# Kernel tuning notes

Hardware: AMD Instinct MI355X
Metric: run time of the kernel (lower is better)

The kernel has to match this reference:

```python
import jax, jax.numpy as jnp
import numpy as np

TOP_K = 2
EPS = 1e-10


def setup_inputs() -> dict:
    key = jax.random.key(0)
    k1, k2 = jax.random.split(key)
    B, S, D, E = 4, 4096, 4096, 64
    hidden_states = jax.random.normal(k1, (B, S, D), dtype=jnp.float32)
    # router weight, scaled like a standard linear init
    w_router = jax.random.normal(k2, (D, E), dtype=jnp.float32) / np.sqrt(D)
    return {"hidden_states": hidden_states, "w_router": w_router}


def reference(hidden_states, w_router):
    # router: [B,S,D] x [D,E] -> [B,S,E]
    router_logits = jnp.einsum("bsd,de->bse", hidden_states, w_router)
    # balanced_assignment: softmax, global load, penalty, adjusted top-k
    routing_probs = jax.nn.softmax(router_logits, axis=-1)
    current_load = routing_probs.sum(axis=(0, 1))            # [E]
    load_penalty = current_load / (current_load.mean() + EPS)  # [E]
    adjusted_logits = router_logits - jnp.log(load_penalty + EPS)
    _, expert_indices = jax.lax.top_k(adjusted_logits, TOP_K)  # [B,S,top_k]
    return adjusted_logits, expert_indices
```

## Files before the change

kernel.cpp:

```cpp
#include <hip/hip_runtime.h>
#include <math.h>

#define ROWS 16384
#define DD   4096
#define EE   64
#define EPSF 1e-10f

#define BM     128
#define KT     32
#define KSPLIT 4
#define KRANGE (DD / KSPLIT)
#define NKT    (KRANGE / KT)
#define WTILE  12288

typedef __attribute__((ext_vector_type(8))) short short8;
typedef __attribute__((ext_vector_type(4))) float f32x4;
typedef __attribute__((ext_vector_type(4))) unsigned u32x4;

__device__ __forceinline__ void split3x8(const float f[8], u32x4& w0,
                                         u32x4& w1, u32x4& w2) {
#pragma unroll
  for (int i = 0; i < 4; ++i) {
    float fa = f[2 * i], fb = f[2 * i + 1];
    unsigned ua = __float_as_uint(fa), ub = __float_as_uint(fb);
    unsigned ra = ua + 0x7fffu + ((ua >> 16) & 1u);
    unsigned rb = ub + 0x7fffu + ((ub >> 16) & 1u);
    w0[i] = (rb & 0xffff0000u) | (ra >> 16);
    fa -= __uint_as_float(ra & 0xffff0000u);
    fb -= __uint_as_float(rb & 0xffff0000u);
    ua = __float_as_uint(fa); ub = __float_as_uint(fb);
    ra = ua + 0x7fffu + ((ua >> 16) & 1u);
    rb = ub + 0x7fffu + ((ub >> 16) & 1u);
    w1[i] = (rb & 0xffff0000u) | (ra >> 16);
    fa -= __uint_as_float(ra & 0xffff0000u);
    fb -= __uint_as_float(rb & 0xffff0000u);
    ua = __float_as_uint(fa); ub = __float_as_uint(fb);
    ra = ua + 0x7fffu + ((ua >> 16) & 1u);
    rb = ub + 0x7fffu + ((ub >> 16) & 1u);
    w2[i] = (rb & 0xffff0000u) | (ra >> 16);
  }
}

__device__ __forceinline__ void dma16(const void* g, void* l) {
  __builtin_amdgcn_global_load_lds(
      (const __attribute__((address_space(1))) unsigned int*)g,
      (__attribute__((address_space(3))) unsigned int*)l, 16, 0, 0);
}

__global__ __launch_bounds__(256) void k_wsplit(const float* __restrict__ wr,
                                                unsigned char* __restrict__ out) {
  const int kt = blockIdx.x;
  const int t = threadIdx.x;
  const int lane = t & 63, wv = t >> 6;
  float f[8];
  const float* wp = wr + (size_t)(kt * 32 + wv * 8) * EE + lane;
#pragma unroll
  for (int j = 0; j < 8; ++j) f[j] = wp[(size_t)j * EE];
  u32x4 w0, w1, w2;
  split3x8(f, w0, w1, w2);
  const int et = lane >> 4;
  const int lp = wv * 16 + (lane & 15);
  unsigned char* base = out + (size_t)kt * WTILE + et * 1024 + lp * 16;
  *(u32x4*)(base + 0 * 4096) = w0;
  *(u32x4*)(base + 1 * 4096) = w1;
  *(u32x4*)(base + 2 * 4096) = w2;
}

__global__ __launch_bounds__(256) void k_gemm(
    const float* __restrict__ h, const unsigned char* __restrict__ wsp,
    float* __restrict__ logits) {
  __shared__ alignas(16) unsigned char wsf[2][WTILE];

  const int t = threadIdx.x;
  const int lane = t & 63;
  const int wv = t >> 6;
  const int row0 = (blockIdx.x >> 2) * BM;
  const int kb0 = (blockIdx.x & 3) * KRANGE;

  f32x4 acc[2][4] = {};

  const int rl0 = row0 + wv * 32 + (lane & 15);
  const int kcol = kb0 + (lane >> 4) * 8;
  const float* ap0 = h + (size_t)rl0 * DD + kcol;
  const float* ap1 = ap0 + (size_t)16 * DD;

  const unsigned char* wsrc = wsp + (size_t)(kb0 / KT) * WTILE;
  const int chunkoff = wv * 1024 + lane * 16;

  float4 cur[4], nxt[4];
  cur[0] = *(const float4*)(ap0);
  cur[1] = *(const float4*)(ap0 + 4);
  cur[2] = *(const float4*)(ap1);
  cur[3] = *(const float4*)(ap1 + 4);
#pragma unroll
  for (int c = 0; c < 3; ++c)
    dma16(wsrc + c * 4096 + chunkoff, &wsf[0][c * 4096 + chunkoff]);

  for (int kt = 0; kt < NKT; ++kt) {
    const int buf = kt & 1;
    asm volatile("s_waitcnt vmcnt(0)" ::: "memory");
    __syncthreads();

    if (kt + 1 < NKT) {
      const float* p0 = ap0 + (size_t)(kt + 1) * KT;
      const float* p1 = ap1 + (size_t)(kt + 1) * KT;
      nxt[0] = *(const float4*)(p0);
      nxt[1] = *(const float4*)(p0 + 4);
      nxt[2] = *(const float4*)(p1);
      nxt[3] = *(const float4*)(p1 + 4);
      const unsigned char* ws = wsrc + (size_t)(kt + 1) * WTILE;
#pragma unroll
      for (int c = 0; c < 3; ++c)
        dma16(ws + c * 4096 + chunkoff, &wsf[buf ^ 1][c * 4096 + chunkoff]);
    }

    short8 bf[3][4];
#pragma unroll
    for (int p = 0; p < 3; ++p)
#pragma unroll
      for (int et = 0; et < 4; ++et)
        bf[p][et] =
            *(const short8*)&wsf[buf][p * 4096 + et * 1024 + lane * 16];

#pragma unroll
    for (int mt = 0; mt < 2; ++mt) {
      const float4 a0 = cur[mt * 2], a1 = cur[mt * 2 + 1];
      const float af[8] = {a0.x, a0.y, a0.z, a0.w, a1.x, a1.y, a1.z, a1.w};
      u32x4 q0, q1, q2;
      split3x8(af, q0, q1, q2);
      const short8 ah0 = __builtin_bit_cast(short8, q0);
      const short8 ah1 = __builtin_bit_cast(short8, q1);
      const short8 ah2 = __builtin_bit_cast(short8, q2);
#pragma unroll
      for (int et = 0; et < 4; ++et) {
        f32x4 c = acc[mt][et];
        c = __builtin_amdgcn_mfma_f32_16x16x32_bf16(ah0, bf[0][et], c, 0, 0, 0);
        c = __builtin_amdgcn_mfma_f32_16x16x32_bf16(ah0, bf[1][et], c, 0, 0, 0);
        c = __builtin_amdgcn_mfma_f32_16x16x32_bf16(ah1, bf[0][et], c, 0, 0, 0);
        c = __builtin_amdgcn_mfma_f32_16x16x32_bf16(ah0, bf[2][et], c, 0, 0, 0);
        c = __builtin_amdgcn_mfma_f32_16x16x32_bf16(ah1, bf[1][et], c, 0, 0, 0);
        c = __builtin_amdgcn_mfma_f32_16x16x32_bf16(ah2, bf[0][et], c, 0, 0, 0);
        acc[mt][et] = c;
      }
    }

    if (kt + 1 < NKT) {
#pragma unroll
      for (int i = 0; i < 4; ++i) cur[i] = nxt[i];
    }
  }

#pragma unroll
  for (int mt = 0; mt < 2; ++mt) {
    const int rbase = row0 + wv * 32 + mt * 16 + (lane >> 4) * 4;
    const int col = lane & 15;
#pragma unroll
    for (int et = 0; et < 4; ++et) {
#pragma unroll
      for (int r = 0; r < 4; ++r)
        atomicAdd(&logits[(size_t)(rbase + r) * EE + et * 16 + col],
                  acc[mt][et][r]);
    }
  }
}

__global__ __launch_bounds__(256) void k_softload(
    const float* __restrict__ logits, float* __restrict__ g_load) {
  __shared__ float red[4][64];
  const int lane = threadIdx.x & 63;
  const int wv = threadIdx.x >> 6;
  float accp = 0.f;
#pragma unroll 4
  for (int i = 0; i < 16; ++i) {
    int row = blockIdx.x * 64 + wv * 16 + i;
    float x = logits[(size_t)row * EE + lane];
    float m = x;
#pragma unroll
    for (int off = 32; off > 0; off >>= 1) m = fmaxf(m, __shfl_xor(m, off, 64));
    float p = __expf(x - m);
    float s = p;
#pragma unroll
    for (int off = 32; off > 0; off >>= 1) s += __shfl_xor(s, off, 64);
    accp += p / s;
  }
  red[wv][lane] = accp;
  __syncthreads();
  if (wv == 0) {
    float s = red[0][lane] + red[1][lane] + red[2][lane] + red[3][lane];
    atomicAdd(&g_load[lane], s);
  }
}

__global__ __launch_bounds__(256) void k_top2(float* __restrict__ logits,
                                              const float* __restrict__ g_load,
                                              float* __restrict__ idx_out) {
  int t = threadIdx.x;
  int lane = t & 63;
  int wv = t >> 6;
  int row = blockIdx.x * 4 + wv;

  float v0 = g_load[lane];
  float s0 = v0;
#pragma unroll
  for (int off = 32; off > 0; off >>= 1) s0 += __shfl_xor(s0, off, 64);
  float lp = logf(v0 / (s0 * (1.f / 64.f) + EPSF) + EPSF);

  size_t base = (size_t)row * EE;
  float a = logits[base + lane] - lp;
  logits[base + lane] = a;

  float v = a;
  int idx = lane;
#pragma unroll
  for (int off = 32; off > 0; off >>= 1) {
    float ov = __shfl_xor(v, off, 64);
    int oi = __shfl_xor(idx, off, 64);
    if (ov > v || (ov == v && oi < idx)) { v = ov; idx = oi; }
  }
  int i1 = idx;

  float a2 = (lane == i1) ? -INFINITY : a;
  v = a2;
  idx = lane;
#pragma unroll
  for (int off = 32; off > 0; off >>= 1) {
    float ov = __shfl_xor(v, off, 64);
    int oi = __shfl_xor(idx, off, 64);
    if (ov > v || (ov == v && oi < idx)) { v = ov; idx = oi; }
  }
  int i2 = idx;

  if (lane == 0) {
    idx_out[(size_t)row * 2 + 0] = (float)i1;
    idx_out[(size_t)row * 2 + 1] = (float)i2;
  }
}

extern "C" void kernel_launch(void* const* d_in, const int* in_sizes, int n_in,
                              void* d_out, int out_size, void* d_ws,
                              size_t ws_size, hipStream_t stream) {
  const float* h = (const float*)d_in[0];
  const float* wr = (const float*)d_in[1];
  float* out = (float*)d_out;
  float* logits = out;
  float* idx_out = out + (size_t)ROWS * EE;
  float* g_load = (float*)d_ws;
  unsigned char* wsp = (unsigned char*)d_ws + 512;

  hipMemsetAsync(d_out, 0, (size_t)ROWS * EE * sizeof(float), stream);
  hipMemsetAsync(d_ws, 0, 512, stream);
  k_wsplit<<<DD / KT, 256, 0, stream>>>(wr, wsp);
  k_gemm<<<(ROWS / BM) * KSPLIT, 256, 0, stream>>>(h, wsp, logits);
  k_softload<<<ROWS / 64, 256, 0, stream>>>(logits, g_load);
  k_top2<<<ROWS / 4, 256, 0, stream>>>(logits, g_load, idx_out);
}
```

Before: 420.1 us.

## Drop split-K, fuse softmax load reduction into GEMM epilogue, remove memsets

```diff
diff --git a/kernel.cpp b/kernel.cpp
--- a/kernel.cpp
+++ b/kernel.cpp
@@ -6,12 +6,10 @@
 #define EE   64
 #define EPSF 1e-10f
 
-#define BM     128
-#define KT     32
-#define KSPLIT 4
-#define KRANGE (DD / KSPLIT)
-#define NKT    (KRANGE / KT)
-#define WTILE  12288
+#define BM    64
+#define KT    32
+#define NKT   (DD / KT)
+#define WTILE 12288
 
 typedef __attribute__((ext_vector_type(8))) short short8;
 typedef __attribute__((ext_vector_type(4))) float f32x4;
@@ -48,10 +46,12 @@
 }
 
 __global__ __launch_bounds__(256) void k_wsplit(const float* __restrict__ wr,
-                                                unsigned char* __restrict__ out) {
+                                                unsigned char* __restrict__ out,
+                                                float* __restrict__ g_load) {
   const int kt = blockIdx.x;
   const int t = threadIdx.x;
   const int lane = t & 63, wv = t >> 6;
+  if (blockIdx.x == 0 && t < 64) g_load[t] = 0.f;
   float f[8];
   const float* wp = wr + (size_t)(kt * 32 + wv * 8) * EE + lane;
 #pragma unroll
@@ -66,127 +66,112 @@
   *(u32x4*)(base + 2 * 4096) = w2;
 }
 
-__global__ __launch_bounds__(256) void k_gemm(
+__global__ __launch_bounds__(512) void k_gemm(
     const float* __restrict__ h, const unsigned char* __restrict__ wsp,
-    float* __restrict__ logits) {
-  __shared__ alignas(16) unsigned char wsf[2][WTILE];
+    float* __restrict__ logits, float* __restrict__ g_load) {
+  __shared__ alignas(16) unsigned char smem[2 * WTILE];
 
   const int t = threadIdx.x;
   const int lane = t & 63;
   const int wv = t >> 6;
-  const int row0 = (blockIdx.x >> 2) * BM;
-  const int kb0 = (blockIdx.x & 3) * KRANGE;
-
-  f32x4 acc[2][4] = {};
-
-  const int rl0 = row0 + wv * 32 + (lane & 15);
-  const int kcol = kb0 + (lane >> 4) * 8;
-  const float* ap0 = h + (size_t)rl0 * DD + kcol;
-  const float* ap1 = ap0 + (size_t)16 * DD;
-
-  const unsigned char* wsrc = wsp + (size_t)(kb0 / KT) * WTILE;
-  const int chunkoff = wv * 1024 + lane * 16;
-
-  float4 cur[4], nxt[4];
-  cur[0] = *(const float4*)(ap0);
-  cur[1] = *(const float4*)(ap0 + 4);
-  cur[2] = *(const float4*)(ap1);
-  cur[3] = *(const float4*)(ap1 + 4);
-#pragma unroll
-  for (int c = 0; c < 3; ++c)
-    dma16(wsrc + c * 4096 + chunkoff, &wsf[0][c * 4096 + chunkoff]);
+  const int mt = wv >> 1;
+  const int eh = wv & 1;
+  const int row0 = blockIdx.x * BM;
+
+  f32x4 acc[2] = {};
+
+  const float* ap =
+      h + (size_t)(row0 + mt * 16 + (lane & 15)) * DD + (lane >> 4) * 8;
+
+  const int slot0 = wv * 1024 + lane * 16;
+
+  float4 cur0, cur1, nxt0, nxt1;
+  cur0 = *(const float4*)(ap);
+  cur1 = *(const float4*)(ap + 4);
+  dma16(wsp + slot0, smem + slot0);
+  if (wv < 4) dma16(wsp + 8192 + slot0, smem + 8192 + slot0);
 
   for (int kt = 0; kt < NKT; ++kt) {
     const int buf = kt & 1;
+    const unsigned char* lb = smem + buf * WTILE;
     asm volatile("s_waitcnt vmcnt(0)" ::: "memory");
     __syncthreads();
 
     if (kt + 1 < NKT) {
-      const float* p0 = ap0 + (size_t)(kt + 1) * KT;
-      const float* p1 = ap1 + (size_t)(kt + 1) * KT;
-      nxt[0] = *(const float4*)(p0);
-      nxt[1] = *(const float4*)(p0 + 4);
-      nxt[2] = *(const float4*)(p1);
-      nxt[3] = *(const float4*)(p1 + 4);
-      const unsigned char* ws = wsrc + (size_t)(kt + 1) * WTILE;
-#pragma unroll
-      for (int c = 0; c < 3; ++c)
-        dma16(ws + c * 4096 + chunkoff, &wsf[buf ^ 1][c * 4096 + chunkoff]);
+      const float* p = ap + (size_t)(kt + 1) * KT;
+      nxt0 = *(const float4*)(p);
+      nxt1 = *(const float4*)(p + 4);
+      const unsigned char* ws = wsp + (size_t)(kt + 1) * WTILE;
+      unsigned char* nb = smem + (buf ^ 1) * WTILE;
+      dma16(ws + slot0, nb + slot0);
+      if (wv < 4) dma16(ws + 8192 + slot0, nb + 8192 + slot0);
     }
 
-    short8 bf[3][4];
+    short8 bf[3][2];
 #pragma unroll
     for (int p = 0; p < 3; ++p)
 #pragma unroll
-      for (int et = 0; et < 4; ++et)
-        bf[p][et] =
-            *(const short8*)&wsf[buf][p * 4096 + et * 1024 + lane * 16];
-
-#pragma unroll
-    for (int mt = 0; mt < 2; ++mt) {
-      const float4 a0 = cur[mt * 2], a1 = cur[mt * 2 + 1];
-      const float af[8] = {a0.x, a0.y, a0.z, a0.w, a1.x, a1.y, a1.z, a1.w};
-      u32x4 q0, q1, q2;
-      split3x8(af, q0, q1, q2);
-      const short8 ah0 = __builtin_bit_cast(short8, q0);
-      const short8 ah1 = __builtin_bit_cast(short8, q1);
-      const short8 ah2 = __builtin_bit_cast(short8, q2);
-#pragma unroll
-      for (int et = 0; et < 4; ++et) {
-        f32x4 c = acc[mt][et];
-        c = __builtin_amdgcn_mfma_f32_16x16x32_bf16(ah0, bf[0][et], c, 0, 0, 0);
-        c = __builtin_amdgcn_mfma_f32_16x16x32_bf16(ah0, bf[1][et], c, 0, 0, 0);
-        c = __builtin_amdgcn_mfma_f32_16x16x32_bf16(ah1, bf[0][et], c, 0, 0, 0);
-        c = __builtin_amdgcn_mfma_f32_16x16x32_bf16(ah0, bf[2][et], c, 0, 0, 0);
-        c = __builtin_amdgcn_mfma_f32_16x16x32_bf16(ah1, bf[1][et], c, 0, 0, 0);
-        c = __builtin_amdgcn_mfma_f32_16x16x32_bf16(ah2, bf[0][et], c, 0, 0, 0);
-        acc[mt][et] = c;
-      }
+      for (int e = 0; e < 2; ++e)
+        bf[p][e] = *(const short8*)&lb[p * 4096 + (eh * 2 + e) * 1024 +
+                                       lane * 16];
+
+    const float af[8] = {cur0.x, cur0.y, cur0.z, cur0.w,
+                         cur1.x, cur1.y, cur1.z, cur1.w};
+    u32x4 q0, q1, q2;
+    split3x8(af, q0, q1, q2);
+    const short8 ah0 = __builtin_bit_cast(short8, q0);
+    const short8 ah1 = __builtin_bit_cast(short8, q1);
+    const short8 ah2 = __builtin_bit_cast(short8, q2);
+#pragma unroll
+    for (int e = 0; e < 2; ++e) {
+      f32x4 c = acc[e];
+      c = __builtin_amdgcn_mfma_f32_16x16x32_bf16(ah0, bf[0][e], c, 0, 0, 0);
+      c = __builtin_amdgcn_mfma_f32_16x16x32_bf16(ah0, bf[1][e], c, 0, 0, 0);
+      c = __builtin_amdgcn_mfma_f32_16x16x32_bf16(ah1, bf[0][e], c, 0, 0, 0);
+      c = __builtin_amdgcn_mfma_f32_16x16x32_bf16(ah0, bf[2][e], c, 0, 0, 0);
+      c = __builtin_amdgcn_mfma_f32_16x16x32_bf16(ah1, bf[1][e], c, 0, 0, 0);
+      c = __builtin_amdgcn_mfma_f32_16x16x32_bf16(ah2, bf[0][e], c, 0, 0, 0);
+      acc[e] = c;
     }
 
-    if (kt + 1 < NKT) {
-#pragma unroll
-      for (int i = 0; i < 4; ++i) cur[i] = nxt[i];
-    }
-  }
-
-#pragma unroll
-  for (int mt = 0; mt < 2; ++mt) {
-    const int rbase = row0 + wv * 32 + mt * 16 + (lane >> 4) * 4;
-    const int col = lane & 15;
-#pragma unroll
-    for (int et = 0; et < 4; ++et) {
+    if (kt + 1 < NKT) { cur0 = nxt0; cur1 = nxt1; }
+  }
+
+  __syncthreads();
+  float* sl = (float*)smem;
+  {
+    const int rb = mt * 16 + (lane >> 4) * 4;
+    const int cb = eh * 32 + (lane & 15);
+#pragma unroll
+    for (int e = 0; e < 2; ++e)
 #pragma unroll
       for (int r = 0; r < 4; ++r)
-        atomicAdd(&logits[(size_t)(rbase + r) * EE + et * 16 + col],
-                  acc[mt][et][r]);
-    }
-  }
-}
-
-__global__ __launch_bounds__(256) void k_softload(
-    const float* __restrict__ logits, float* __restrict__ g_load) {
-  __shared__ float red[4][64];
-  const int lane = threadIdx.x & 63;
-  const int wv = threadIdx.x >> 6;
+        sl[(rb + r) * 68 + cb + e * 16] = acc[e][r];
+  }
+  __syncthreads();
+
   float accp = 0.f;
-#pragma unroll 4
-  for (int i = 0; i < 16; ++i) {
-    int row = blockIdx.x * 64 + wv * 16 + i;
-    float x = logits[(size_t)row * EE + lane];
+#pragma unroll
+  for (int i = 0; i < 8; ++i) {
+    const int row = wv * 8 + i;
+    const float x = sl[row * 68 + lane];
     float m = x;
 #pragma unroll
     for (int off = 32; off > 0; off >>= 1) m = fmaxf(m, __shfl_xor(m, off, 64));
-    float p = __expf(x - m);
+    const float p = __expf(x - m);
     float s = p;
 #pragma unroll
     for (int off = 32; off > 0; off >>= 1) s += __shfl_xor(s, off, 64);
     accp += p / s;
-  }
-  red[wv][lane] = accp;
+    logits[(size_t)(row0 + row) * EE + lane] = x;
+  }
+  float* red = sl + 64 * 68;
+  red[wv * 64 + lane] = accp;
   __syncthreads();
   if (wv == 0) {
-    float s = red[0][lane] + red[1][lane] + red[2][lane] + red[3][lane];
+    float s = 0.f;
+#pragma unroll
+    for (int j = 0; j < 8; ++j) s += red[j * 64 + lane];
     atomicAdd(&g_load[lane], s);
   }
 }
@@ -247,10 +232,7 @@
   float* g_load = (float*)d_ws;
   unsigned char* wsp = (unsigned char*)d_ws + 512;
 
-  hipMemsetAsync(d_out, 0, (size_t)ROWS * EE * sizeof(float), stream);
-  hipMemsetAsync(d_ws, 0, 512, stream);
-  k_wsplit<<<DD / KT, 256, 0, stream>>>(wr, wsp);
-  k_gemm<<<(ROWS / BM) * KSPLIT, 256, 0, stream>>>(h, wsp, logits);
-  k_softload<<<ROWS / 64, 256, 0, stream>>>(logits, g_load);
+  k_wsplit<<<DD / KT, 256, 0, stream>>>(wr, wsp, g_load);
+  k_gemm<<<ROWS / BM, 512, 0, stream>>>(h, wsp, logits, g_load);
   k_top2<<<ROWS / 4, 256, 0, stream>>>(logits, g_load, idx_out);
 }
```

New measurement: 449.6 us. 1.07x slower.
